# Optimization experiments

Hardware: AMD Instinct MI355X
Metric: run time of the kernel (lower is better)

The kernel has to match this reference:

```python
import jax, jax.numpy as jnp
import numpy as np

B, C, H, W = 2, 256, 64, 64
HEADS, DIM_HEAD = 8, 64
INNER = HEADS * DIM_HEAD


def setup_inputs() -> dict:
    key = jax.random.key(0)
    k1, k2, k3, k4 = jax.random.split(key, 4)
    x = jax.random.normal(k1, (B, C, H, W), dtype=jnp.float32)
    # 1x1 conv weights stored as [out_ch, in_ch]
    w_qkv = jax.random.normal(k2, (3 * INNER, C), dtype=jnp.float32) * (1.0 / np.sqrt(C))
    w_out = jax.random.normal(k3, (C, INNER), dtype=jnp.float32) * (1.0 / np.sqrt(INNER))
    b_out = jax.random.normal(k4, (C,), dtype=jnp.float32) * 0.01
    return {"x": x, "w_qkv": w_qkv, "w_out": w_out, "b_out": b_out}


def reference(x, w_qkv, w_out, b_out):
    b, c, h, w = x.shape
    n = h * w
    # 1x1 conv == channel matmul
    qkv = jnp.einsum('oc,bchw->bohw', w_qkv, x)  # [B, 3*inner, H, W]
    qkv = qkv.reshape(b, 3, HEADS, DIM_HEAD, n)
    qkv = jnp.transpose(qkv, (1, 0, 2, 4, 3))    # [3, B, heads, N, dim_head]
    q, k, v = qkv[0], qkv[1], qkv[2]
    scale = 1.0 / (DIM_HEAD ** 0.5)
    dots = jnp.einsum('bhnd,bhmd->bhnm', q, k) * scale  # [B, heads, N, N]
    attn = jax.nn.softmax(dots, axis=-1)
    out = jnp.einsum('bhnm,bhmd->bhnd', attn, v)        # [B, heads, N, dim_head]
    out = jnp.transpose(out, (0, 1, 3, 2)).reshape(b, INNER, h, w)
    return jnp.einsum('ci,bihw->bchw', w_out, out) + b_out[None, :, None, None]
```

## Files before the change

kernel.cpp:

```cpp
#include <hip/hip_runtime.h>
#include <hip/hip_bf16.h>

typedef unsigned short u16;
typedef __attribute__((ext_vector_type(8))) short bf16x8;
typedef __attribute__((ext_vector_type(4))) short bf16x4;
typedef __attribute__((ext_vector_type(4))) float f32x4;
typedef __attribute__((ext_vector_type(8))) unsigned short u16x8;
typedef __attribute__((ext_vector_type(4))) unsigned short u16x4;

#define N_POS 4096
#define HEADS 8
#define DHEAD 64
#define CIN   256
#define INNER 512
#define NSPLIT 2
#define JCHUNK (N_POS / NSPLIT)

__device__ __forceinline__ u16 f2bf(float f) {
    union { float f; unsigned int u; } v; v.f = f;
    unsigned int u = v.u + 0x7FFFu + ((v.u >> 16) & 1u);
    return (u16)(u >> 16);
}

__device__ __forceinline__ unsigned int pkbf2(float lo, float hi) {
    union { __hip_bfloat162 b; unsigned int u; } cv;
    cv.b = __float22bfloat162_rn(make_float2(lo, hi));
    return cv.u;
}

__global__ __launch_bounds__(256) void k0_prep(const float* __restrict__ x,
                                               const float* __restrict__ w_qkv,
                                               const float* __restrict__ w_out,
                                               u16* __restrict__ xT,
                                               u16* __restrict__ wq,
                                               u16* __restrict__ wo) {
    int bid = blockIdx.x;
    int t   = threadIdx.x;
    if (bid < 256) {
        int b = bid >> 7, rest = bid & 127;
        int n  = (rest & 15) * 256 + t;
        int c0 = (rest >> 4) * 32;
        const float* xp = x + (size_t)b * CIN * N_POS + n;
        u16* op = xT + ((size_t)(b * N_POS + n)) * CIN + c0;
        for (int g = 0; g < 4; ++g) {
            u16x8 v;
            for (int j = 0; j < 8; ++j)
                v[j] = f2bf(xp[(size_t)(c0 + g * 8 + j) * N_POS]);
            *(u16x8*)(op + g * 8) = v;
        }
    } else if (bid < 448) {
        size_t idx = (size_t)(bid - 256) * 2048 + t * 8;
        u16x8 v;
        for (int j = 0; j < 8; ++j) v[j] = f2bf(w_qkv[idx + j]);
        *(u16x8*)(wq + idx) = v;
    } else {
        size_t idx = (size_t)(bid - 448) * 2048 + t * 8;
        u16x8 v;
        for (int j = 0; j < 8; ++j) v[j] = f2bf(w_out[idx + j]);
        *(u16x8*)(wo + idx) = v;
    }
}

__global__ __launch_bounds__(256, 4) void k1_qkv(const u16* __restrict__ wq,
                                                 const u16* __restrict__ xT,
                                                 u16* __restrict__ q_ws,
                                                 u16* __restrict__ k_ws,
                                                 u16* __restrict__ vt_ws) {
    __shared__ u16 Alds[64 * 40];
    __shared__ u16 Blds[128 * 40];
    int tid = threadIdx.x;
    int n0  = blockIdx.x * 128;
    int by  = blockIdx.y;
    int b   = blockIdx.z;
    int o0  = by * 64;
    int sel = by >> 3;
    int h   = by & 7;
    int wv = tid >> 6, l = tid & 63, quad = l >> 4, l15 = l & 15;
    int srow = tid >> 2, sseg = tid & 3;
    int brow = tid >> 1, bseg = tid & 1;

    f32x4 acc[8] = {};
    for (int c0 = 0; c0 < CIN; c0 += 32) {
        *(u16x8*)&Alds[srow * 40 + sseg * 8] =
            *(const u16x8*)(wq + (size_t)(o0 + srow) * CIN + c0 + sseg * 8);
        const u16* xp = xT + ((size_t)(b * N_POS + n0 + brow)) * CIN + c0 + bseg * 16;
        *(u16x8*)&Blds[brow * 40 + bseg * 16]     = *(const u16x8*)xp;
        *(u16x8*)&Blds[brow * 40 + bseg * 16 + 8] = *(const u16x8*)(xp + 8);
        __syncthreads();
        bf16x8 af = *(const bf16x8*)&Alds[(wv * 16 + l15) * 40 + quad * 8];
        for (int nt = 0; nt < 8; ++nt) {
            bf16x8 bfrag = *(const bf16x8*)&Blds[(nt * 16 + l15) * 40 + quad * 8];
            acc[nt] = __builtin_amdgcn_mfma_f32_16x16x32_bf16(af, bfrag, acc[nt], 0, 0, 0);
        }
        __syncthreads();
    }
    const float QSCALE = 0.125f * 1.44269504088896f;
    float sc = (sel == 0) ? QSCALE : 1.0f;
    int dbase = wv * 16 + quad * 4;
    for (int nt = 0; nt < 8; ++nt) {
        int n = n0 + nt * 16 + l15;
        if (sel < 2) {
            u16* base = (sel == 0) ? q_ws : k_ws;
            u16x4 pk;
            for (int r = 0; r < 4; ++r) pk[r] = f2bf(acc[nt][r] * sc);
            *(u16x4*)&base[((size_t)((b * HEADS + h) * N_POS + n)) * DHEAD + dbase] = pk;
        } else {
            for (int r = 0; r < 4; ++r)
                vt_ws[((size_t)((b * HEADS + h) * DHEAD + dbase + r)) * N_POS + n] =
                    f2bf(acc[nt][r]);
        }
    }
}

__global__ __launch_bounds__(256, 4) void k2_attn(const u16* __restrict__ q_ws,
                                                  const u16* __restrict__ k_ws,
                                                  const u16* __restrict__ vt_ws,
                                                  float* __restrict__ op_ws,
                                                  float* __restrict__ lw_ws) {
    __shared__ u16 Klds[64 * 72];
    __shared__ u16 Vlds[64 * 72];
    int tid = threadIdx.x;
    int q0  = blockIdx.x * 128;
    int bh  = blockIdx.y;
    int half = blockIdx.z;
    int jbase = half * JCHUNK;
    int wv = tid >> 6, l = tid & 63, quad = l >> 4, l15 = l & 15;
    int srow = tid >> 2, sseg = tid & 3;

    const u16* qp = q_ws + ((size_t)(bh * N_POS + q0 + wv * 32 + l15)) * DHEAD + quad * 8;
    bf16x8 bq[2][2];
    bq[0][0] = *(const bf16x8*)qp;
    bq[0][1] = *(const bf16x8*)(qp + 32);
    bq[1][0] = *(const bf16x8*)(qp + 16 * DHEAD);
    bq[1][1] = *(const bf16x8*)(qp + 16 * DHEAD + 32);

    f32x4 Oacc[2][4] = {};
    float lsum[2] = {0.f, 0.f};

    const u16* kp = k_ws + ((size_t)(bh * N_POS + srow)) * DHEAD + sseg * 16;
    const u16* vp = vt_ws + ((size_t)(bh * DHEAD + srow)) * N_POS + sseg * 16;

    u16x8 pf0 = *(const u16x8*)(kp + (size_t)jbase * DHEAD);
    u16x8 pf1 = *(const u16x8*)(kp + (size_t)jbase * DHEAD + 8);
    u16x8 pf2 = *(const u16x8*)(vp + jbase);
    u16x8 pf3 = *(const u16x8*)(vp + jbase + 8);

    for (int j0 = jbase; j0 < jbase + JCHUNK; j0 += 64) {
        *(u16x8*)&Klds[srow * 72 + sseg * 16]     = pf0;
        *(u16x8*)&Klds[srow * 72 + sseg * 16 + 8] = pf1;
        *(u16x8*)&Vlds[srow * 72 + sseg * 16]     = pf2;
        *(u16x8*)&Vlds[srow * 72 + sseg * 16 + 8] = pf3;
        __syncthreads();

        if (j0 + 64 < jbase + JCHUNK) {
            const u16* kpj = kp + (size_t)(j0 + 64) * DHEAD;
            pf0 = *(const u16x8*)kpj;
            pf1 = *(const u16x8*)(kpj + 8);
            pf2 = *(const u16x8*)(vp + j0 + 64);
            pf3 = *(const u16x8*)(vp + j0 + 72);
        }

        f32x4 ST[2][4];
        for (int jt = 0; jt < 4; ++jt) {
            const u16* kb = &Klds[(jt * 16 + l15) * 72 + quad * 8];
            bf16x8 kf0 = *(const bf16x8*)kb;
            bf16x8 kf1 = *(const bf16x8*)(kb + 32);
            for (int it = 0; it < 2; ++it) {
                f32x4 z = {};
                z = __builtin_amdgcn_mfma_f32_16x16x32_bf16(kf0, bq[it][0], z, 0, 0, 0);
                z = __builtin_amdgcn_mfma_f32_16x16x32_bf16(kf1, bq[it][1], z, 0, 0, 0);
                ST[it][jt] = z;
            }
        }

        bf16x4 pk[2][4];
        for (int it = 0; it < 2; ++it) {
            float rs = 0.f;
            for (int jt = 0; jt < 4; ++jt)
                for (int r = 0; r < 4; ++r) {
                    float p = __builtin_amdgcn_exp2f(ST[it][jt][r]);
                    ST[it][jt][r] = p;
                    rs += p;
                }
            lsum[it] += rs;
            for (int jt = 0; jt < 4; ++jt) {
                union { unsigned int u[2]; bf16x4 v; } cv;
                cv.u[0] = pkbf2(ST[it][jt][0], ST[it][jt][1]);
                cv.u[1] = pkbf2(ST[it][jt][2], ST[it][jt][3]);
                pk[it][jt] = cv.v;
            }
        }

        for (int dt = 0; dt < 4; ++dt) {
            const u16* vb = &Vlds[(dt * 16 + l15) * 72 + quad * 4];
            for (int jt = 0; jt < 4; ++jt) {
                bf16x4 vf = *(const bf16x4*)(vb + jt * 16);
                Oacc[0][dt] = __builtin_amdgcn_mfma_f32_16x16x16bf16_1k(vf, pk[0][jt], Oacc[0][dt], 0, 0, 0);
                Oacc[1][dt] = __builtin_amdgcn_mfma_f32_16x16x16bf16_1k(vf, pk[1][jt], Oacc[1][dt], 0, 0, 0);
            }
        }
        __syncthreads();
    }

    int b = bh >> 3, h = bh & 7;
    float* opb = op_ws + (size_t)half * 2 * N_POS * INNER;
    float* lwb = lw_ws + (size_t)half * 2 * HEADS * N_POS;
    for (int it = 0; it < 2; ++it) {
        float ls = lsum[it];
        ls += __shfl_xor(ls, 16);
        ls += __shfl_xor(ls, 32);
        int n = q0 + wv * 32 + it * 16 + l15;
        if (quad == 0) lwb[(size_t)bh * N_POS + n] = ls;
        float* dst = opb + ((size_t)(b * N_POS + n)) * INNER + h * DHEAD;
        for (int dt = 0; dt < 4; ++dt)
            *(f32x4*)&dst[dt * 16 + quad * 4] = Oacc[it][dt];
    }
}

__global__ __launch_bounds__(256) void k2c_combine(const float* __restrict__ op_ws,
                                                   const float* __restrict__ lw_ws,
                                                   u16* __restrict__ ao_ws) {
    size_t gid = (size_t)blockIdx.x * 256 + threadIdx.x;
    size_t e0  = gid * 16;
    int i0 = (int)(e0 & (INNER - 1));
    size_t nf = e0 >> 9;
    int h = i0 >> 6;
    size_t b = nf >> 12;
    size_t n = nf & (N_POS - 1);
    size_t lidx = (b * HEADS + h) * N_POS + n;
    float ls = lw_ws[lidx] + lw_ws[(size_t)2 * HEADS * N_POS + lidx];
    float inv = 1.0f / ls;
    const float* p0 = op_ws + e0;
    const float* p1 = op_ws + (size_t)2 * N_POS * INNER + e0;
    u16x8 o[2];
    for (int g = 0; g < 2; ++g) {
        for (int k = 0; k < 8; ++k) {
            int idx = g * 8 + k;
            o[g][k] = f2bf((p0[idx] + p1[idx]) * inv);
        }
    }
    *(u16x8*)(ao_ws + e0)     = o[0];
    *(u16x8*)(ao_ws + e0 + 8) = o[1];
}

__global__ __launch_bounds__(256) void k3_out(const u16* __restrict__ wo,
                                              const float* __restrict__ b_out,
                                              const u16* __restrict__ ao_ws,
                                              float* __restrict__ out) {
    __shared__ u16 Alds[64 * 40];
    __shared__ u16 Blds[64 * 40];
    int tid = threadIdx.x;
    int n0 = blockIdx.x * 64;
    int c0 = blockIdx.y * 64;
    int b  = blockIdx.z;
    int wv = tid >> 6, l = tid & 63, quad = l >> 4, l15 = l & 15;
    int srow = tid >> 2, sseg = tid & 3;

    f32x4 acc[4] = {};
    for (int i0 = 0; i0 < INNER; i0 += 32) {
        *(u16x8*)&Alds[srow * 40 + sseg * 8] =
            *(const u16x8*)(wo + (size_t)(c0 + srow) * INNER + i0 + sseg * 8);
        *(u16x8*)&Blds[srow * 40 + sseg * 8] =
            *(const u16x8*)(ao_ws + ((size_t)(b * N_POS + n0 + srow)) * INNER + i0 + sseg * 8);
        __syncthreads();
        bf16x8 af = *(const bf16x8*)&Alds[(wv * 16 + l15) * 40 + quad * 8];
        for (int nt = 0; nt < 4; ++nt) {
            bf16x8 bfrag = *(const bf16x8*)&Blds[(nt * 16 + l15) * 40 + quad * 8];
            acc[nt] = __builtin_amdgcn_mfma_f32_16x16x32_bf16(af, bfrag, acc[nt], 0, 0, 0);
        }
        __syncthreads();
    }
    for (int r = 0; r < 4; ++r) {
        int c = c0 + wv * 16 + quad * 4 + r;
        float bias = b_out[c];
        for (int nt = 0; nt < 4; ++nt) {
            int n = n0 + nt * 16 + l15;
            out[((size_t)(b * CIN + c)) * N_POS + n] = acc[nt][r] + bias;
        }
    }
}

extern "C" void kernel_launch(void* const* d_in, const int* in_sizes, int n_in,
                              void* d_out, int out_size, void* d_ws, size_t ws_size,
                              hipStream_t stream) {
    const float* x     = (const float*)d_in[0];
    const float* w_qkv = (const float*)d_in[1];
    const float* w_out = (const float*)d_in[2];
    const float* b_out = (const float*)d_in[3];
    float* out = (float*)d_out;

    u16* ws    = (u16*)d_ws;
    u16* xT    = ws;
    u16* q_ws  = xT   + (size_t)2 * N_POS * CIN;
    u16* k_ws  = q_ws + (size_t)2 * HEADS * N_POS * DHEAD;
    u16* vt_ws = k_ws + (size_t)2 * HEADS * N_POS * DHEAD;
    u16* ao_ws = vt_ws + (size_t)2 * HEADS * N_POS * DHEAD;
    u16* wq_bf = ao_ws + (size_t)2 * N_POS * INNER;
    u16* wo_bf = wq_bf + (size_t)3 * INNER * CIN;
    float* op_ws = (float*)(wo_bf + (size_t)CIN * INNER);
    float* lw_ws = op_ws + (size_t)NSPLIT * 2 * N_POS * INNER;

    hipLaunchKernelGGL(k0_prep, dim3(512), dim3(256), 0, stream,
                       x, w_qkv, w_out, xT, wq_bf, wo_bf);
    hipLaunchKernelGGL(k1_qkv, dim3(32, 24, 2), dim3(256), 0, stream,
                       wq_bf, xT, q_ws, k_ws, vt_ws);
    hipLaunchKernelGGL(k2_attn, dim3(32, 16, NSPLIT), dim3(256), 0, stream,
                       q_ws, k_ws, vt_ws, op_ws, lw_ws);
    hipLaunchKernelGGL(k2c_combine, dim3((2 * N_POS * INNER) / (256 * 16)), dim3(256), 0, stream,
                       op_ws, lw_ws, ao_ws);
    hipLaunchKernelGGL(k3_out, dim3(64, 4, 2), dim3(256), 0, stream,
                       wo_bf, b_out, ao_ws, out);
}
```

Measured before the change: 193.9 us.

## Enlarge attention query tile, use K=32 MFMA for PV, fuse combine into output GEMM

The attention kernel now processes 256 queries per block (64 per wave) instead of 128, so each K/V tile staged in LDS is reused by twice as many queries. K rows are permuted on store so the P fragments from the QK^T MFMA can feed the 16x16x32 bf16 MFMA for P·V directly, replacing the 16x16x16 variant. The separate combine kernel is removed: k3_out now reads both split partials and the row sums, normalises and converts to bf16 while loading its B tile. This cuts one launch and a workspace round trip, but doubles register pressure in k2_attn (launch bounds lowered to 2), halves the attention grid, and repeats the combine work in each of the four c-blocks of k3_out.

```diff
diff --git a/kernel.cpp b/kernel.cpp
--- a/kernel.cpp
+++ b/kernel.cpp
@@ -3,7 +3,6 @@
 
 typedef unsigned short u16;
 typedef __attribute__((ext_vector_type(8))) short bf16x8;
-typedef __attribute__((ext_vector_type(4))) short bf16x4;
 typedef __attribute__((ext_vector_type(4))) float f32x4;
 typedef __attribute__((ext_vector_type(8))) unsigned short u16x8;
 typedef __attribute__((ext_vector_type(4))) unsigned short u16x4;
@@ -112,7 +111,7 @@
     }
 }
 
-__global__ __launch_bounds__(256, 4) void k2_attn(const u16* __restrict__ q_ws,
+__global__ __launch_bounds__(256, 2) void k2_attn(const u16* __restrict__ q_ws,
                                                   const u16* __restrict__ k_ws,
                                                   const u16* __restrict__ vt_ws,
                                                   float* __restrict__ op_ws,
@@ -120,22 +119,23 @@
     __shared__ u16 Klds[64 * 72];
     __shared__ u16 Vlds[64 * 72];
     int tid = threadIdx.x;
-    int q0  = blockIdx.x * 128;
+    int q0  = blockIdx.x * 256;
     int bh  = blockIdx.y;
     int half = blockIdx.z;
     int jbase = half * JCHUNK;
     int wv = tid >> 6, l = tid & 63, quad = l >> 4, l15 = l & 15;
     int srow = tid >> 2, sseg = tid & 3;
-
-    const u16* qp = q_ws + ((size_t)(bh * N_POS + q0 + wv * 32 + l15)) * DHEAD + quad * 8;
-    bf16x8 bq[2][2];
-    bq[0][0] = *(const bf16x8*)qp;
-    bq[0][1] = *(const bf16x8*)(qp + 32);
-    bq[1][0] = *(const bf16x8*)(qp + 16 * DHEAD);
-    bq[1][1] = *(const bf16x8*)(qp + 16 * DHEAD + 32);
-
-    f32x4 Oacc[2][4] = {};
-    float lsum[2] = {0.f, 0.f};
+    int srowp = (srow & 0x23) | ((srow & 4) << 2) | ((srow & 0x18) >> 1);
+
+    const u16* qp = q_ws + ((size_t)(bh * N_POS + q0 + wv * 64 + l15)) * DHEAD + quad * 8;
+    bf16x8 bq[4][2];
+    for (int it = 0; it < 4; ++it) {
+        bq[it][0] = *(const bf16x8*)(qp + (size_t)it * 16 * DHEAD);
+        bq[it][1] = *(const bf16x8*)(qp + (size_t)it * 16 * DHEAD + 32);
+    }
+
+    f32x4 Oacc[4][4] = {};
+    float lsum[4] = {0.f, 0.f, 0.f, 0.f};
 
     const u16* kp = k_ws + ((size_t)(bh * N_POS + srow)) * DHEAD + sseg * 16;
     const u16* vp = vt_ws + ((size_t)(bh * DHEAD + srow)) * N_POS + sseg * 16;
@@ -146,10 +146,10 @@
     u16x8 pf3 = *(const u16x8*)(vp + jbase + 8);
 
     for (int j0 = jbase; j0 < jbase + JCHUNK; j0 += 64) {
-        *(u16x8*)&Klds[srow * 72 + sseg * 16]     = pf0;
-        *(u16x8*)&Klds[srow * 72 + sseg * 16 + 8] = pf1;
-        *(u16x8*)&Vlds[srow * 72 + sseg * 16]     = pf2;
-        *(u16x8*)&Vlds[srow * 72 + sseg * 16 + 8] = pf3;
+        *(u16x8*)&Klds[srowp * 72 + sseg * 16]     = pf0;
+        *(u16x8*)&Klds[srowp * 72 + sseg * 16 + 8] = pf1;
+        *(u16x8*)&Vlds[srow * 72 + sseg * 16]      = pf2;
+        *(u16x8*)&Vlds[srow * 72 + sseg * 16 + 8]  = pf3;
         __syncthreads();
 
         if (j0 + 64 < jbase + JCHUNK) {
@@ -160,56 +160,51 @@
             pf3 = *(const u16x8*)(vp + j0 + 72);
         }
 
-        f32x4 ST[2][4];
-        for (int jt = 0; jt < 4; ++jt) {
-            const u16* kb = &Klds[(jt * 16 + l15) * 72 + quad * 8];
-            bf16x8 kf0 = *(const bf16x8*)kb;
-            bf16x8 kf1 = *(const bf16x8*)(kb + 32);
-            for (int it = 0; it < 2; ++it) {
-                f32x4 z = {};
-                z = __builtin_amdgcn_mfma_f32_16x16x32_bf16(kf0, bq[it][0], z, 0, 0, 0);
-                z = __builtin_amdgcn_mfma_f32_16x16x32_bf16(kf1, bq[it][1], z, 0, 0, 0);
-                ST[it][jt] = z;
+        unsigned int pkw[4][2][4];
+        for (int p = 0; p < 2; ++p)
+            for (int a = 0; a < 2; ++a) {
+                const u16* kb = &Klds[((2 * p + a) * 16 + l15) * 72 + quad * 8];
+                bf16x8 kf0 = *(const bf16x8*)kb;
+                bf16x8 kf1 = *(const bf16x8*)(kb + 32);
+                f32x4 z[4];
+                for (int it = 0; it < 4; ++it) {
+                    f32x4 t = {};
+                    t = __builtin_amdgcn_mfma_f32_16x16x32_bf16(kf0, bq[it][0], t, 0, 0, 0);
+                    t = __builtin_amdgcn_mfma_f32_16x16x32_bf16(kf1, bq[it][1], t, 0, 0, 0);
+                    z[it] = t;
+                }
+                for (int it = 0; it < 4; ++it) {
+                    float e0 = __builtin_amdgcn_exp2f(z[it][0]);
+                    float e1 = __builtin_amdgcn_exp2f(z[it][1]);
+                    float e2 = __builtin_amdgcn_exp2f(z[it][2]);
+                    float e3 = __builtin_amdgcn_exp2f(z[it][3]);
+                    lsum[it] += (e0 + e1) + (e2 + e3);
+                    pkw[it][p][2 * a]     = pkbf2(e0, e1);
+                    pkw[it][p][2 * a + 1] = pkbf2(e2, e3);
+                }
             }
-        }
-
-        bf16x4 pk[2][4];
-        for (int it = 0; it < 2; ++it) {
-            float rs = 0.f;
-            for (int jt = 0; jt < 4; ++jt)
-                for (int r = 0; r < 4; ++r) {
-                    float p = __builtin_amdgcn_exp2f(ST[it][jt][r]);
-                    ST[it][jt][r] = p;
-                    rs += p;
+
+        for (int dt = 0; dt < 4; ++dt)
+            for (int p = 0; p < 2; ++p) {
+                bf16x8 vf = *(const bf16x8*)&Vlds[(dt * 16 + l15) * 72 + p * 32 + quad * 8];
+                for (int it = 0; it < 4; ++it) {
+                    union { unsigned int u[4]; bf16x8 v; } cv;
+                    cv.u[0] = pkw[it][p][0]; cv.u[1] = pkw[it][p][1];
+                    cv.u[2] = pkw[it][p][2]; cv.u[3] = pkw[it][p][3];
+                    Oacc[it][dt] = __builtin_amdgcn_mfma_f32_16x16x32_bf16(vf, cv.v, Oacc[it][dt], 0, 0, 0);
                 }
-            lsum[it] += rs;
-            for (int jt = 0; jt < 4; ++jt) {
-                union { unsigned int u[2]; bf16x4 v; } cv;
-                cv.u[0] = pkbf2(ST[it][jt][0], ST[it][jt][1]);
-                cv.u[1] = pkbf2(ST[it][jt][2], ST[it][jt][3]);
-                pk[it][jt] = cv.v;
             }
-        }
-
-        for (int dt = 0; dt < 4; ++dt) {
-            const u16* vb = &Vlds[(dt * 16 + l15) * 72 + quad * 4];
-            for (int jt = 0; jt < 4; ++jt) {
-                bf16x4 vf = *(const bf16x4*)(vb + jt * 16);
-                Oacc[0][dt] = __builtin_amdgcn_mfma_f32_16x16x16bf16_1k(vf, pk[0][jt], Oacc[0][dt], 0, 0, 0);
-                Oacc[1][dt] = __builtin_amdgcn_mfma_f32_16x16x16bf16_1k(vf, pk[1][jt], Oacc[1][dt], 0, 0, 0);
-            }
-        }
         __syncthreads();
     }
 
     int b = bh >> 3, h = bh & 7;
     float* opb = op_ws + (size_t)half * 2 * N_POS * INNER;
     float* lwb = lw_ws + (size_t)half * 2 * HEADS * N_POS;
-    for (int it = 0; it < 2; ++it) {
+    for (int it = 0; it < 4; ++it) {
         float ls = lsum[it];
         ls += __shfl_xor(ls, 16);
         ls += __shfl_xor(ls, 32);
-        int n = q0 + wv * 32 + it * 16 + l15;
+        int n = q0 + wv * 64 + it * 16 + l15;
         if (quad == 0) lwb[(size_t)bh * N_POS + n] = ls;
         float* dst = opb + ((size_t)(b * N_POS + n)) * INNER + h * DHEAD;
         for (int dt = 0; dt < 4; ++dt)
@@ -217,35 +212,10 @@
     }
 }
 
-__global__ __launch_bounds__(256) void k2c_combine(const float* __restrict__ op_ws,
-                                                   const float* __restrict__ lw_ws,
-                                                   u16* __restrict__ ao_ws) {
-    size_t gid = (size_t)blockIdx.x * 256 + threadIdx.x;
-    size_t e0  = gid * 16;
-    int i0 = (int)(e0 & (INNER - 1));
-    size_t nf = e0 >> 9;
-    int h = i0 >> 6;
-    size_t b = nf >> 12;
-    size_t n = nf & (N_POS - 1);
-    size_t lidx = (b * HEADS + h) * N_POS + n;
-    float ls = lw_ws[lidx] + lw_ws[(size_t)2 * HEADS * N_POS + lidx];
-    float inv = 1.0f / ls;
-    const float* p0 = op_ws + e0;
-    const float* p1 = op_ws + (size_t)2 * N_POS * INNER + e0;
-    u16x8 o[2];
-    for (int g = 0; g < 2; ++g) {
-        for (int k = 0; k < 8; ++k) {
-            int idx = g * 8 + k;
-            o[g][k] = f2bf((p0[idx] + p1[idx]) * inv);
-        }
-    }
-    *(u16x8*)(ao_ws + e0)     = o[0];
-    *(u16x8*)(ao_ws + e0 + 8) = o[1];
-}
-
 __global__ __launch_bounds__(256) void k3_out(const u16* __restrict__ wo,
                                               const float* __restrict__ b_out,
-                                              const u16* __restrict__ ao_ws,
+                                              const float* __restrict__ op_ws,
+                                              const float* __restrict__ lw_ws,
                                               float* __restrict__ out) {
     __shared__ u16 Alds[64 * 40];
     __shared__ u16 Blds[64 * 40];
@@ -260,8 +230,22 @@
     for (int i0 = 0; i0 < INNER; i0 += 32) {
         *(u16x8*)&Alds[srow * 40 + sseg * 8] =
             *(const u16x8*)(wo + (size_t)(c0 + srow) * INNER + i0 + sseg * 8);
-        *(u16x8*)&Blds[srow * 40 + sseg * 8] =
-            *(const u16x8*)(ao_ws + ((size_t)(b * N_POS + n0 + srow)) * INNER + i0 + sseg * 8);
+        {
+            int i = i0 + sseg * 8;
+            int h = i >> 6;
+            int n = n0 + srow;
+            size_t lidx = ((size_t)(b * HEADS + h)) * N_POS + n;
+            float ls = lw_ws[lidx] + lw_ws[(size_t)2 * HEADS * N_POS + lidx];
+            float inv = 1.0f / ls;
+            const float* p0 = op_ws + ((size_t)(b * N_POS + n)) * INNER + i;
+            const float* p1 = p0 + (size_t)2 * N_POS * INNER;
+            f32x4 a0 = *(const f32x4*)p0, a1 = *(const f32x4*)(p0 + 4);
+            f32x4 b0 = *(const f32x4*)p1, b1 = *(const f32x4*)(p1 + 4);
+            u16x8 v;
+            for (int k = 0; k < 4; ++k) v[k]     = f2bf((a0[k] + b0[k]) * inv);
+            for (int k = 0; k < 4; ++k) v[4 + k] = f2bf((a1[k] + b1[k]) * inv);
+            *(u16x8*)&Blds[srow * 40 + sseg * 8] = v;
+        }
         __syncthreads();
         bf16x8 af = *(const bf16x8*)&Alds[(wv * 16 + l15) * 40 + quad * 8];
         for (int nt = 0; nt < 4; ++nt) {
@@ -294,8 +278,7 @@
     u16* q_ws  = xT   + (size_t)2 * N_POS * CIN;
     u16* k_ws  = q_ws + (size_t)2 * HEADS * N_POS * DHEAD;
     u16* vt_ws = k_ws + (size_t)2 * HEADS * N_POS * DHEAD;
-    u16* ao_ws = vt_ws + (size_t)2 * HEADS * N_POS * DHEAD;
-    u16* wq_bf = ao_ws + (size_t)2 * N_POS * INNER;
+    u16* wq_bf = vt_ws + (size_t)2 * HEADS * N_POS * DHEAD;
     u16* wo_bf = wq_bf + (size_t)3 * INNER * CIN;
     float* op_ws = (float*)(wo_bf + (size_t)CIN * INNER);
     float* lw_ws = op_ws + (size_t)NSPLIT * 2 * N_POS * INNER;
@@ -304,10 +287,8 @@
                        x, w_qkv, w_out, xT, wq_bf, wo_bf);
     hipLaunchKernelGGL(k1_qkv, dim3(32, 24, 2), dim3(256), 0, stream,
                        wq_bf, xT, q_ws, k_ws, vt_ws);
-    hipLaunchKernelGGL(k2_attn, dim3(32, 16, NSPLIT), dim3(256), 0, stream,
+    hipLaunchKernelGGL(k2_attn, dim3(16, 16, NSPLIT), dim3(256), 0, stream,
                        q_ws, k_ws, vt_ws, op_ws, lw_ws);
-    hipLaunchKernelGGL(k2c_combine, dim3((2 * N_POS * INNER) / (256 * 16)), dim3(256), 0, stream,
-                       op_ws, lw_ws, ao_ws);
     hipLaunchKernelGGL(k3_out, dim3(64, 4, 2), dim3(256), 0, stream,
-                       wo_bf, b_out, ao_ws, out);
-}
+                       wo_bf, b_out, op_ws, lw_ws, out);
+}
```

New measurement: 178.7 us. 7.9% less time.
